# Optimization experiments

Hardware: AMD Instinct MI355X
Metric: run time of the kernel (lower is better)

## Reference

```python
import jax, jax.numpy as jnp
import numpy as np

DECAY = 0.99
EPS = 1e-05
N_EMBED = 4096

def setup_inputs() -> dict:
    key = jax.random.key(0)
    k1, k2 = jax.random.split(key)
    x = jax.random.normal(k1, (32, 1024, 256), dtype=jnp.float32)
    embed = jax.random.normal(k2, (256, N_EMBED), dtype=jnp.float32)
    cluster_size = jnp.zeros((N_EMBED,), dtype=jnp.float32)
    embed_avg = embed  # buffer initialized as embed.clone()
    return {"x": x, "embed": embed, "cluster_size": cluster_size, "embed_avg": embed_avg}

def reference(x, embed, cluster_size, embed_avg):
    # x: [B, L, D]; embed/embed_avg: [D, K]; cluster_size: [K]
    B, L, D = x.shape
    K = embed.shape[1]
    flat = x.reshape(B * L, D)
    dist = (jnp.sum(flat * flat, axis=1, keepdims=True)
            - 2.0 * flat @ embed
            + jnp.sum(embed * embed, axis=0, keepdims=True))
    embed_indices = jnp.argmin(dist, axis=1)  # [N]
    # one-hot scatter-sum (counts per code)
    embed_onehot_sum = jnp.zeros((K,), dtype=x.dtype).at[embed_indices].add(1.0)
    # EMA updates, faithful to the torch source including its quirks:
    #   cluster_size.mul_(decay).add_(onehot_sum, alpha=1-eps)  (note: 1-eps, not 1-decay)
    #   embed_avg.mul_(decay).add(embed_sum, ...)  -> .add (not in-place), so embed_sum is discarded
    cluster_size_new = cluster_size * DECAY + embed_onehot_sum * (1.0 - EPS)
    embed_avg_new = embed_avg * DECAY
    n = jnp.sum(cluster_size_new)
    cs = (cluster_size_new + EPS) / (n + K * EPS) * n  # Laplace-smoothed counts
    embed_new = embed_avg_new / cs[None, :]  # [D, K], copied into self.embed before lookup
    # codebook lookup with the UPDATED embed (matches embed.data.copy_ ordering)
    quantize = embed_new.T[embed_indices].reshape(B, L, D)
    diff = jnp.mean(jnp.square(jax.lax.stop_gradient(quantize) - x))
    quantize_st = x + jax.lax.stop_gradient(quantize - x)  # straight-through
    return (quantize_st, embed_indices.reshape(B, L), diff,
            cluster_size_new, embed_avg_new, embed_new)
```

## Files before the change

### kernel.cpp

```cpp
#include <hip/hip_runtime.h>
#include <math.h>

constexpr float DECAY = 0.99f;
constexpr float EPS_F = 1e-5f;
constexpr float MARGIN = 0.08f;

typedef short bf16x8 __attribute__((ext_vector_type(8)));
typedef float f32x4 __attribute__((ext_vector_type(4)));
typedef float vf4 __attribute__((ext_vector_type(4)));

#define BM 128
#define KSPLIT 2
#define NU 128
#define D_FIX 256

__device__ __forceinline__ unsigned rne_bf16(float f) {
  unsigned u = __float_as_uint(f);
  return (u + 0x7fffu + ((u >> 16) & 1u)) >> 16;
}
__device__ __forceinline__ unsigned pack_hilo(float v) {
  unsigned u = __float_as_uint(v);
  unsigned hi = u & 0xffff0000u;
  float rem = v - __uint_as_float(hi);
  return hi | rne_bf16(rem);
}

__global__ void k_prepack(const float* __restrict__ e, ushort* __restrict__ phl, int K) {
  __shared__ ushort tile[8192];
  const int unit = blockIdx.x;
  const int ct = unit >> 2, du = unit & 3;
  const int t = threadIdx.x;
#pragma unroll
  for (int p = 0; p < 16; ++p) {
    int idx = t + p * 256;
    int dl = idx >> 6, col = idx & 63;
    float v = e[(size_t)(du * 64 + dl) * K + ct * 64 + col];
    unsigned pk = pack_hilo(v);
    int pos = col * 64 + (((dl >> 3) ^ (col & 7)) << 3) + (dl & 7);
    tile[pos] = (ushort)(pk >> 16);
    tile[4096 + pos] = (ushort)(pk & 0xffffu);
  }
  __syncthreads();
  uint4* dst = (uint4*)(phl + (size_t)unit * 8192);
  const uint4* srcT = (const uint4*)tile;
#pragma unroll
  for (int p = 0; p < 4; ++p) dst[t + p * 256] = srcT[t + p * 256];
}

__global__ void k_enorm(const float* __restrict__ e, double* __restrict__ e2d,
                        float* __restrict__ e2f, int D, int K) {
  __shared__ double red[4][64];
  const int kl = threadIdx.x & 63;
  const int part = threadIdx.x >> 6;
  const int k = blockIdx.x * 64 + kl;
  double s = 0.0;
  for (int d = part; d < D; d += 4) {
    double v = (double)e[(size_t)d * K + k];
    s = fma(v, v, s);
  }
  red[part][kl] = s;
  __syncthreads();
  if (part == 0) {
    double t = ((red[0][kl] + red[1][kl]) + red[2][kl]) + red[3][kl];
    e2d[k] = t;
    e2f[k] = (float)t;
  }
}

__launch_bounds__(256, 2)
__global__ void k_argmin_mfma(const float* __restrict__ x, const ushort* __restrict__ phl,
                              const float* __restrict__ e2f,
                              float* __restrict__ bestv, float* __restrict__ secv,
                              int* __restrict__ besti, int N, int K) {
  __shared__ ushort es[2][8192];
  __shared__ float e2s[2048];

  const int tid = threadIdx.x;
  const int w   = tid >> 6;
  const int l   = tid & 63;
  const int g   = l >> 4;
  const int c16 = l & 15;

  const int bflat = blockIdx.x + gridDim.x * blockIdx.y;
  const int xcd   = bflat & 7;
  const int slot  = bflat >> 3;
  const int ytile = xcd >> 2;
  const int xtile = (xcd & 3) * (gridDim.x >> 2) + slot;

  const int kbase = ytile * (K / KSPLIT);
  const int rowW  = xtile * BM + w * 32;

  char* esb = (char*)es;

#define STAGE(u_, b_) do {                                                          \
    const char* gs_ = (const char*)phl +                                            \
        (((size_t)ytile * NU + (size_t)(u_)) << 14) + (w << 12) + (l << 4);         \
    char* ld_ = esb + ((b_) << 14) + (w << 12);                                     \
    __builtin_amdgcn_global_load_lds((const unsigned*)(gs_),        (unsigned*)(ld_),        16, 0, 0); \
    __builtin_amdgcn_global_load_lds((const unsigned*)(gs_ + 1024), (unsigned*)(ld_ + 1024), 16, 0, 0); \
    __builtin_amdgcn_global_load_lds((const unsigned*)(gs_ + 2048), (unsigned*)(ld_ + 2048), 16, 0, 0); \
    __builtin_amdgcn_global_load_lds((const unsigned*)(gs_ + 3072), (unsigned*)(ld_ + 3072), 16, 0, 0); \
  } while (0)

  STAGE(0, 0);

  for (int i = tid; i < 2048; i += 256) e2s[i] = e2f[kbase + i];

  bf16x8 xh[2][8], xl[2][8];
#pragma unroll
  for (int m = 0; m < 2; ++m) {
    const float* xr = x + (size_t)(rowW + m * 16 + c16) * D_FIX + 8 * g;
#pragma unroll
    for (int t = 0; t < 8; ++t) {
      vf4 fa = __builtin_nontemporal_load((const vf4*)(xr + t * 32));
      vf4 fb = __builtin_nontemporal_load((const vf4*)(xr + t * 32 + 4));
      float f[8] = {fa.x, fa.y, fa.z, fa.w, fb.x, fb.y, fb.z, fb.w};
      union { unsigned u[4]; bf16x8 v; } H, L;
#pragma unroll
      for (int p = 0; p < 4; ++p) {
        unsigned w0 = pack_hilo(f[2 * p]);
        unsigned w1 = pack_hilo(f[2 * p + 1]);
        H.u[p] = (w0 >> 16) | (w1 & 0xffff0000u);
        L.u[p] = (w0 & 0xffffu) | (w1 << 16);
      }
      xh[m][t] = H.v;
      xl[m][t] = L.v;
    }
  }

  float best[2][4], sec[2][4];
  int bidx[2][4];
#pragma unroll
  for (int m = 0; m < 2; ++m)
#pragma unroll
    for (int r = 0; r < 4; ++r) { best[m][r] = 3e38f; sec[m][r] = 3e38f; bidx[m][r] = 0; }

  const int sw16 = ((g ^ (c16 & 7)) << 4);
  const char* thr0 = esb + c16 * 128;

  f32x4 acc[2][4];

  for (int u = 0; u < NU; ++u) {
    __syncthreads();
    if (u + 1 < NU) STAGE(u + 1, (u + 1) & 1);
    const int kt = u >> 2, du = u & 3;

    if (du == 0) {
#pragma unroll
      for (int m = 0; m < 2; ++m)
#pragma unroll
        for (int c = 0; c < 4; ++c) acc[m][c] = (f32x4){0.f, 0.f, 0.f, 0.f};
    }

    const char* pbuf = thr0 + ((u & 1) << 14);
#pragma unroll
    for (int tt = 0; tt < 2; ++tt) {
      const int t = 2 * du + tt;
      const char* pt = pbuf + (sw16 ^ (tt << 6));
#pragma unroll
      for (int c = 0; c < 4; ++c) {
        bf16x8 bh = *(const bf16x8*)(pt + c * 2048);
        bf16x8 bl = *(const bf16x8*)(pt + c * 2048 + 8192);
#pragma unroll
        for (int m = 0; m < 2; ++m) {
          acc[m][c] = __builtin_amdgcn_mfma_f32_16x16x32_bf16(xh[m][t], bh, acc[m][c], 0, 0, 0);
          acc[m][c] = __builtin_amdgcn_mfma_f32_16x16x32_bf16(xh[m][t], bl, acc[m][c], 0, 0, 0);
          acc[m][c] = __builtin_amdgcn_mfma_f32_16x16x32_bf16(xl[m][t], bh, acc[m][c], 0, 0, 0);
        }
      }
    }

    if (du == 3) {
#pragma unroll
      for (int c = 0; c < 4; ++c) {
        const int klocal = kt * 64 + c * 16 + c16;
        const float e2v = e2s[klocal];
        const int kg = kbase + klocal;
#pragma unroll
        for (int m = 0; m < 2; ++m)
#pragma unroll
          for (int r = 0; r < 4; ++r) {
            float dist = fmaf(-2.f, acc[m][c][r], e2v);
            if (dist < best[m][r]) { sec[m][r] = best[m][r]; best[m][r] = dist; bidx[m][r] = kg; }
            else sec[m][r] = fminf(sec[m][r], dist);
          }
      }
    }
  }
#undef STAGE

#pragma unroll
  for (int off = 1; off < 16; off <<= 1) {
#pragma unroll
    for (int m = 0; m < 2; ++m)
#pragma unroll
      for (int r = 0; r < 4; ++r) {
        float ob = __shfl_xor(best[m][r], off);
        float os = __shfl_xor(sec[m][r], off);
        int   oi = __shfl_xor(bidx[m][r], off);
        if (ob < best[m][r] || (ob == best[m][r] && oi < bidx[m][r])) {
          sec[m][r] = fminf(best[m][r], os); best[m][r] = ob; bidx[m][r] = oi;
        } else {
          sec[m][r] = fminf(sec[m][r], ob);
        }
      }
  }

  if (c16 == 0) {
    const size_t base = (size_t)ytile * N;
#pragma unroll
    for (int m = 0; m < 2; ++m)
#pragma unroll
      for (int r = 0; r < 4; ++r) {
        int row = rowW + m * 16 + 4 * g + r;
        bestv[base + row] = best[m][r];
        secv[base + row]  = sec[m][r];
        besti[base + row] = bidx[m][r];
      }
  }
}

__global__ void k_combine(const float* __restrict__ bestv, const float* __restrict__ secv,
                          const int* __restrict__ besti, int* __restrict__ idx_out,
                          int* __restrict__ list, unsigned int* __restrict__ count, int N) {
  int n = blockIdx.x * blockDim.x + threadIdx.x;
  if (n >= N) return;
  float b = bestv[n], s = secv[n];
  int bi = besti[n];
#pragma unroll
  for (int p = 1; p < KSPLIT; ++p) {
    float ob = bestv[(size_t)p * N + n];
    float os = secv[(size_t)p * N + n];
    int   oi = besti[(size_t)p * N + n];
    if (ob < b || (ob == b && oi < bi)) { s = fminf(b, os); b = ob; bi = oi; }
    else s = fminf(s, ob);
  }
  idx_out[n] = bi;
  if (s - b < MARGIN) {
    unsigned int p = atomicAdd(count, 1u);
    list[p] = n;
  }
}

__launch_bounds__(256, 4)
__global__ void k_rescan(const float* __restrict__ x, const float* __restrict__ e,
                         const double* __restrict__ e2d, const int* __restrict__ list,
                         const unsigned int* __restrict__ count, int* __restrict__ idx_out,
                         int K) {
  __shared__ double xrow[D_FIX];
  __shared__ double rv[256];
  __shared__ int ri[256];
  const int tid = threadIdx.x;
  const unsigned int cnt = *count;
  for (unsigned int ii = blockIdx.x; ii < cnt; ii += gridDim.x) {
    const int row = list[ii];
    __syncthreads();
    xrow[tid] = (double)x[(size_t)row * D_FIX + tid];
    __syncthreads();
    double bb = 1e300; int bi = 0;
    for (int j = 0; j < K; j += 256) {
      const int k = j + tid;
      const float* ek = e + k;
      double a0 = 0.0, a1 = 0.0, a2 = 0.0, a3 = 0.0;
#pragma unroll 8
      for (int d = 0; d < D_FIX; d += 4) {
        a0 = fma(xrow[d + 0], (double)ek[(size_t)(d + 0) * K], a0);
        a1 = fma(xrow[d + 1], (double)ek[(size_t)(d + 1) * K], a1);
        a2 = fma(xrow[d + 2], (double)ek[(size_t)(d + 2) * K], a2);
        a3 = fma(xrow[d + 3], (double)ek[(size_t)(d + 3) * K], a3);
      }
      double dist = e2d[k] - 2.0 * ((a0 + a1) + (a2 + a3));
      if (dist < bb || (dist == bb && k < bi)) { bb = dist; bi = k; }
    }
    rv[tid] = bb; ri[tid] = bi;
    __syncthreads();
    for (int off = 128; off > 0; off >>= 1) {
      if (tid < off) {
        if (rv[tid + off] < rv[tid] || (rv[tid + off] == rv[tid] && ri[tid + off] < ri[tid])) {
          rv[tid] = rv[tid + off]; ri[tid] = ri[tid + off];
        }
      }
      __syncthreads();
    }
    if (tid == 0) idx_out[row] = ri[0];
    __syncthreads();
  }
}

__global__ void k_hist(const int* __restrict__ idx, unsigned int* __restrict__ cnt,
                       float* __restrict__ idxf_out, int N) {
  int n = blockIdx.x * blockDim.x + threadIdx.x;
  if (n >= N) return;
  int c = idx[n];
  idxf_out[n] = (float)c;
  atomicAdd(&cnt[c], 1u);
}

__global__ void k_cluster(const float* __restrict__ cs_in,
                          const unsigned int* __restrict__ cnt,
                          float* __restrict__ out_csn, float* __restrict__ cs_ws,
                          int K) {
  __shared__ double red[256];
  const int tid = threadIdx.x;
  double s = 0.0;
  for (int k = tid; k < K; k += 256) {
    float csn = cs_in[k] * DECAY + (float)cnt[k] * (1.0f - EPS_F);
    out_csn[k] = csn;
    s += (double)csn;
  }
  red[tid] = s;
  __syncthreads();
  for (int off = 128; off > 0; off >>= 1) {
    if (tid < off) red[tid] += red[tid + off];
    __syncthreads();
  }
  const float n = (float)red[0];
  const float denom = n + (float)K * EPS_F;
  for (int k = tid; k < K; k += 256) {
    float csn = out_csn[k];
    cs_ws[k] = (csn + EPS_F) / denom * n;
  }
}

__global__ void k_embed(const float* __restrict__ avg_in, const float* __restrict__ cs_ws,
                        float* __restrict__ out_avg, float* __restrict__ out_emb, int K) {
  int k = blockIdx.x * blockDim.x + threadIdx.x;
  int d = blockIdx.y;
  if (k >= K) return;
  size_t i = (size_t)d * K + k;
  float a = avg_in[i] * DECAY;
  out_avg[i] = a;
  out_emb[i] = a / cs_ws[k];
}

__global__ void k_transpose(const float* __restrict__ src, float* __restrict__ dst,
                            int D, int K) {
  __shared__ float t[64][65];
  const int kb = blockIdx.x * 64;
  const int db = blockIdx.y * 64;
  const int c = threadIdx.x & 63;
  const int r0 = (threadIdx.x >> 6) * 16;
  for (int i = 0; i < 16; ++i)
    t[r0 + i][c] = src[(size_t)(db + r0 + i) * K + kb + c];
  __syncthreads();
  for (int i = 0; i < 16; ++i)
    dst[(size_t)(kb + r0 + i) * D + db + c] = t[c][r0 + i];
}

__global__ void k_gather(const float* __restrict__ x, const float* __restrict__ embT,
                         const int* __restrict__ idx, float* __restrict__ out_q,
                         float* __restrict__ partial) {
  __shared__ float red[256];
  const int tid = threadIdx.x;
  const int n0 = blockIdx.x * 64;
  float s = 0.f;
  for (int u = 0; u < 16; ++u) {
    int i = u * 256 + tid;
    int row = n0 + (i >> 6);
    int f4 = (i & 63) * 4;
    int code = idx[row];
    float4 q  = *(const float4*)&embT[(size_t)code * D_FIX + f4];
    float4 xv = *(const float4*)&x[(size_t)row * D_FIX + f4];
    float4 dv = {q.x - xv.x, q.y - xv.y, q.z - xv.z, q.w - xv.w};
    float4 val = {xv.x + dv.x, xv.y + dv.y, xv.z + dv.z, xv.w + dv.w};
    *(float4*)&out_q[(size_t)row * D_FIX + f4] = val;
    s += dv.x * dv.x + dv.y * dv.y + dv.z * dv.z + dv.w * dv.w;
  }
  red[tid] = s;
  __syncthreads();
  for (int off = 128; off > 0; off >>= 1) {
    if (tid < off) red[tid] += red[tid + off];
    __syncthreads();
  }
  if (tid == 0) partial[blockIdx.x] = red[0];
}

__global__ void k_diff(const float* __restrict__ partial, float* __restrict__ out_diff,
                       int NB, long long total) {
  __shared__ double red[256];
  const int tid = threadIdx.x;
  double s = 0.0;
  for (int i = tid; i < NB; i += 256) s += (double)partial[i];
  red[tid] = s;
  __syncthreads();
  for (int off = 128; off > 0; off >>= 1) {
    if (tid < off) red[tid] += red[tid + off];
    __syncthreads();
  }
  if (tid == 0) out_diff[0] = (float)(red[0] / (double)total);
}

extern "C" void kernel_launch(void* const* d_in, const int* in_sizes, int n_in,
                              void* d_out, int out_size, void* d_ws, size_t ws_size,
                              hipStream_t stream) {
  const float* x            = (const float*)d_in[0];
  const float* embed        = (const float*)d_in[1];
  const float* cluster_size = (const float*)d_in[2];
  const float* embed_avg    = (const float*)d_in[3];

  const int K = in_sizes[2];
  const int D = in_sizes[1] / K;
  const int N = in_sizes[0] / D;

  float* out      = (float*)d_out;
  float* out_q    = out;
  float* out_idx  = out_q + (size_t)N * D;
  float* out_diff = out_idx + N;
  float* out_csn  = out_diff + 1;
  float* out_avg  = out_csn + K;
  float* out_emb  = out_avg + (size_t)D * K;

  char* ws = (char*)d_ws;
  double*       e2d     = (double*)ws;               ws += (size_t)K * 8;
  float*        e2f     = (float*)ws;                ws += (size_t)K * 4;
  int*          idx     = (int*)ws;                  ws += (size_t)N * 4;
  unsigned int* cnt     = (unsigned int*)ws;         ws += (size_t)K * 4;
  float*        cs_ws   = (float*)ws;                ws += (size_t)K * 4;
  float*        partial = (float*)ws;                ws += (size_t)(N / 64) * 4;
  float*        bestv   = (float*)ws;                ws += (size_t)KSPLIT * N * 4;
  float*        secv    = (float*)ws;                ws += (size_t)KSPLIT * N * 4;
  int*          besti   = (int*)ws;                  ws += (size_t)KSPLIT * N * 4;
  int*          list    = (int*)ws;                  ws += (size_t)N * 4;
  unsigned int* count   = (unsigned int*)ws;         ws += 64;
  float*        embT    = (float*)ws;                ws += (size_t)K * D * 4;
  ushort*       phl     = (ushort*)ws;               ws += (size_t)K * D * 4;

  hipMemsetAsync(cnt, 0, (size_t)K * sizeof(unsigned int), stream);
  hipMemsetAsync(count, 0, sizeof(unsigned int), stream);

  k_prepack<<<dim3((K / 64) * 4), dim3(256), 0, stream>>>(embed, phl, K);
  k_enorm<<<dim3(K / 64), dim3(256), 0, stream>>>(embed, e2d, e2f, D, K);
  k_argmin_mfma<<<dim3(N / BM, KSPLIT), dim3(256), 0, stream>>>(x, phl, e2f, bestv, secv,
                                                                besti, N, K);
  k_combine<<<dim3((N + 255) / 256), dim3(256), 0, stream>>>(bestv, secv, besti, idx,
                                                             list, count, N);
  k_rescan<<<dim3(1024), dim3(256), 0, stream>>>(x, embed, e2d, list, count, idx, K);
  k_hist<<<dim3((N + 255) / 256), dim3(256), 0, stream>>>(idx, cnt, out_idx, N);
  k_cluster<<<dim3(1), dim3(256), 0, stream>>>(cluster_size, cnt, out_csn, cs_ws, K);
  k_embed<<<dim3((K + 255) / 256, D), dim3(256), 0, stream>>>(embed_avg, cs_ws, out_avg, out_emb, K);
  k_transpose<<<dim3(K / 64, D / 64), dim3(256), 0, stream>>>(out_emb, embT, D, K);
  k_gather<<<dim3(N / 64), dim3(256), 0, stream>>>(x, embT, idx, out_q, partial);
  k_diff<<<dim3(1), dim3(256), 0, stream>>>(partial, out_diff, N / 64, (long long)N * D);
}
```

Before: 510.3 us.

## Deepen argmin pipeline, widen blocks, and fuse auxiliary kernels

The MFMA argmin kernel now uses 512-thread blocks covering 256 rows and a 6-deep LDS ring with explicit vmcnt waits instead of double buffering, so more codebook tiles are in flight. Prepack and norm are merged into one kernel, the histogram is folded into combine and rescan, and the embed update is fused with the transpose. The packed codebook now lives in the out_avg output region instead of separate workspace, relying on it being overwritten later. These changes cut kernel launches and extra passes, at the cost of larger LDS use and tighter correctness dependencies on the buffer-reuse ordering.

```diff
diff --git a/kernel.cpp b/kernel.cpp
--- a/kernel.cpp
+++ b/kernel.cpp
@@ -9,9 +9,10 @@
 typedef float f32x4 __attribute__((ext_vector_type(4)));
 typedef float vf4 __attribute__((ext_vector_type(4)));
 
-#define BM 128
+#define BM 256
 #define KSPLIT 2
 #define NU 128
+#define NBUF 6
 #define D_FIX 256
 
 __device__ __forceinline__ unsigned rne_bf16(float f) {
@@ -25,59 +26,58 @@
   return hi | rne_bf16(rem);
 }
 
-__global__ void k_prepack(const float* __restrict__ e, ushort* __restrict__ phl, int K) {
+__global__ void k_prepack_enorm(const float* __restrict__ e, ushort* __restrict__ phl,
+                                double* __restrict__ e2d, float* __restrict__ e2f, int K) {
   __shared__ ushort tile[8192];
-  const int unit = blockIdx.x;
-  const int ct = unit >> 2, du = unit & 3;
+  __shared__ double red[4][64];
+  const int ct = blockIdx.x;
   const int t = threadIdx.x;
-#pragma unroll
-  for (int p = 0; p < 16; ++p) {
-    int idx = t + p * 256;
-    int dl = idx >> 6, col = idx & 63;
-    float v = e[(size_t)(du * 64 + dl) * K + ct * 64 + col];
-    unsigned pk = pack_hilo(v);
-    int pos = col * 64 + (((dl >> 3) ^ (col & 7)) << 3) + (dl & 7);
-    tile[pos] = (ushort)(pk >> 16);
-    tile[4096 + pos] = (ushort)(pk & 0xffffu);
-  }
-  __syncthreads();
-  uint4* dst = (uint4*)(phl + (size_t)unit * 8192);
-  const uint4* srcT = (const uint4*)tile;
-#pragma unroll
-  for (int p = 0; p < 4; ++p) dst[t + p * 256] = srcT[t + p * 256];
-}
-
-__global__ void k_enorm(const float* __restrict__ e, double* __restrict__ e2d,
-                        float* __restrict__ e2f, int D, int K) {
-  __shared__ double red[4][64];
-  const int kl = threadIdx.x & 63;
-  const int part = threadIdx.x >> 6;
-  const int k = blockIdx.x * 64 + kl;
+  for (int du = 0; du < 4; ++du) {
+    __syncthreads();
+#pragma unroll
+    for (int p = 0; p < 16; ++p) {
+      int idx = t + p * 256;
+      int dl = idx >> 6, col = idx & 63;
+      float v = e[(size_t)(du * 64 + dl) * K + ct * 64 + col];
+      unsigned pk = pack_hilo(v);
+      int pos = col * 64 + (((dl >> 3) ^ (col & 7)) << 3) + (dl & 7);
+      tile[pos] = (ushort)(pk >> 16);
+      tile[4096 + pos] = (ushort)(pk & 0xffffu);
+    }
+    __syncthreads();
+    uint4* dst = (uint4*)(phl + (size_t)(ct * 4 + du) * 8192);
+    const uint4* srcT = (const uint4*)tile;
+#pragma unroll
+    for (int p = 0; p < 4; ++p) dst[t + p * 256] = srcT[t + p * 256];
+  }
+  const int kl = t & 63;
+  const int part = t >> 6;
+  const int k = ct * 64 + kl;
   double s = 0.0;
-  for (int d = part; d < D; d += 4) {
+  for (int d = part; d < D_FIX; d += 4) {
     double v = (double)e[(size_t)d * K + k];
     s = fma(v, v, s);
   }
   red[part][kl] = s;
   __syncthreads();
   if (part == 0) {
-    double t = ((red[0][kl] + red[1][kl]) + red[2][kl]) + red[3][kl];
-    e2d[k] = t;
-    e2f[k] = (float)t;
-  }
-}
-
-__launch_bounds__(256, 2)
+    double tt = ((red[0][kl] + red[1][kl]) + red[2][kl]) + red[3][kl];
+    e2d[k] = tt;
+    e2f[k] = (float)tt;
+  }
+}
+
+__launch_bounds__(512, 2)
 __global__ void k_argmin_mfma(const float* __restrict__ x, const ushort* __restrict__ phl,
                               const float* __restrict__ e2f,
                               float* __restrict__ bestv, float* __restrict__ secv,
                               int* __restrict__ besti, int N, int K) {
-  __shared__ ushort es[2][8192];
+  __shared__ ushort es[NBUF][8192];
   __shared__ float e2s[2048];
 
   const int tid = threadIdx.x;
+  const int l   = tid & 63;
   const int w   = tid >> 6;
-  const int l   = tid & 63;
   const int g   = l >> 4;
   const int c16 = l & 15;
 
@@ -91,20 +91,16 @@
   const int rowW  = xtile * BM + w * 32;
 
   char* esb = (char*)es;
-
-#define STAGE(u_, b_) do {                                                          \
-    const char* gs_ = (const char*)phl +                                            \
-        (((size_t)ytile * NU + (size_t)(u_)) << 14) + (w << 12) + (l << 4);         \
-    char* ld_ = esb + ((b_) << 14) + (w << 12);                                     \
-    __builtin_amdgcn_global_load_lds((const unsigned*)(gs_),        (unsigned*)(ld_),        16, 0, 0); \
-    __builtin_amdgcn_global_load_lds((const unsigned*)(gs_ + 1024), (unsigned*)(ld_ + 1024), 16, 0, 0); \
-    __builtin_amdgcn_global_load_lds((const unsigned*)(gs_ + 2048), (unsigned*)(ld_ + 2048), 16, 0, 0); \
-    __builtin_amdgcn_global_load_lds((const unsigned*)(gs_ + 3072), (unsigned*)(ld_ + 3072), 16, 0, 0); \
-  } while (0)
-
-  STAGE(0, 0);
-
-  for (int i = tid; i < 2048; i += 256) e2s[i] = e2f[kbase + i];
+  const size_t unit0 = (size_t)ytile * NU;
+
+  auto stage = [&](int u) {
+    const char* gs = (const char*)phl + ((unit0 + (size_t)u) << 14) + (w << 11) + (l << 4);
+    char* ld = esb + ((u % NBUF) << 14) + (w << 11) + (l << 4);
+    __builtin_amdgcn_global_load_lds((const unsigned*)gs,          (unsigned*)ld,          16, 0, 0);
+    __builtin_amdgcn_global_load_lds((const unsigned*)(gs + 1024), (unsigned*)(ld + 1024), 16, 0, 0);
+  };
+
+  for (int i = tid; i < 2048; i += 512) e2s[i] = e2f[kbase + i];
 
   bf16x8 xh[2][8], xl[2][8];
 #pragma unroll
@@ -136,23 +132,19 @@
     for (int r = 0; r < 4; ++r) { best[m][r] = 3e38f; sec[m][r] = 3e38f; bidx[m][r] = 0; }
 
   const int sw16 = ((g ^ (c16 & 7)) << 4);
-  const char* thr0 = esb + c16 * 128;
+  const int c16x128 = c16 * 128;
 
   f32x4 acc[2][4];
 
-  for (int u = 0; u < NU; ++u) {
-    __syncthreads();
-    if (u + 1 < NU) STAGE(u + 1, (u + 1) & 1);
+  auto compute = [&](int u) {
     const int kt = u >> 2, du = u & 3;
-
     if (du == 0) {
 #pragma unroll
       for (int m = 0; m < 2; ++m)
 #pragma unroll
         for (int c = 0; c < 4; ++c) acc[m][c] = (f32x4){0.f, 0.f, 0.f, 0.f};
     }
-
-    const char* pbuf = thr0 + ((u & 1) << 14);
+    const char* pbuf = esb + ((u % NBUF) << 14) + c16x128;
 #pragma unroll
     for (int tt = 0; tt < 2; ++tt) {
       const int t = 2 * du + tt;
@@ -169,7 +161,6 @@
         }
       }
     }
-
     if (du == 3) {
 #pragma unroll
       for (int c = 0; c < 4; ++c) {
@@ -186,8 +177,32 @@
           }
       }
     }
-  }
-#undef STAGE
+  };
+
+  __syncthreads();
+  stage(0); stage(1); stage(2); stage(3); stage(4);
+
+  for (int u = 0; u < NU - 5; ++u) {
+    asm volatile("s_waitcnt vmcnt(8)" ::: "memory");
+    __builtin_amdgcn_s_barrier();
+    stage(u + 5);
+    compute(u);
+  }
+  asm volatile("s_waitcnt vmcnt(8)" ::: "memory");
+  __builtin_amdgcn_s_barrier();
+  compute(NU - 5);
+  asm volatile("s_waitcnt vmcnt(6)" ::: "memory");
+  __builtin_amdgcn_s_barrier();
+  compute(NU - 4);
+  asm volatile("s_waitcnt vmcnt(4)" ::: "memory");
+  __builtin_amdgcn_s_barrier();
+  compute(NU - 3);
+  asm volatile("s_waitcnt vmcnt(2)" ::: "memory");
+  __builtin_amdgcn_s_barrier();
+  compute(NU - 2);
+  asm volatile("s_waitcnt vmcnt(0)" ::: "memory");
+  __builtin_amdgcn_s_barrier();
+  compute(NU - 1);
 
 #pragma unroll
   for (int off = 1; off < 16; off <<= 1) {
@@ -222,6 +237,7 @@
 
 __global__ void k_combine(const float* __restrict__ bestv, const float* __restrict__ secv,
                           const int* __restrict__ besti, int* __restrict__ idx_out,
+                          float* __restrict__ idxf_out, unsigned int* __restrict__ cnt,
                           int* __restrict__ list, unsigned int* __restrict__ count, int N) {
   int n = blockIdx.x * blockDim.x + threadIdx.x;
   if (n >= N) return;
@@ -236,9 +252,12 @@
     else s = fminf(s, ob);
   }
   idx_out[n] = bi;
+  idxf_out[n] = (float)bi;
   if (s - b < MARGIN) {
     unsigned int p = atomicAdd(count, 1u);
     list[p] = n;
+  } else {
+    atomicAdd(&cnt[bi], 1u);
   }
 }
 
@@ -246,13 +265,14 @@
 __global__ void k_rescan(const float* __restrict__ x, const float* __restrict__ e,
                          const double* __restrict__ e2d, const int* __restrict__ list,
                          const unsigned int* __restrict__ count, int* __restrict__ idx_out,
+                         float* __restrict__ idxf_out, unsigned int* __restrict__ cnt,
                          int K) {
   __shared__ double xrow[D_FIX];
   __shared__ double rv[256];
   __shared__ int ri[256];
   const int tid = threadIdx.x;
-  const unsigned int cnt = *count;
-  for (unsigned int ii = blockIdx.x; ii < cnt; ii += gridDim.x) {
+  const unsigned int cntN = *count;
+  for (unsigned int ii = blockIdx.x; ii < cntN; ii += gridDim.x) {
     const int row = list[ii];
     __syncthreads();
     xrow[tid] = (double)x[(size_t)row * D_FIX + tid];
@@ -282,18 +302,13 @@
       }
       __syncthreads();
     }
-    if (tid == 0) idx_out[row] = ri[0];
-    __syncthreads();
-  }
-}
-
-__global__ void k_hist(const int* __restrict__ idx, unsigned int* __restrict__ cnt,
-                       float* __restrict__ idxf_out, int N) {
-  int n = blockIdx.x * blockDim.x + threadIdx.x;
-  if (n >= N) return;
-  int c = idx[n];
-  idxf_out[n] = (float)c;
-  atomicAdd(&cnt[c], 1u);
+    if (tid == 0) {
+      idx_out[row] = ri[0];
+      idxf_out[row] = (float)ri[0];
+      atomicAdd(&cnt[ri[0]], 1u);
+    }
+    __syncthreads();
+  }
 }
 
 __global__ void k_cluster(const float* __restrict__ cs_in,
@@ -322,29 +337,26 @@
   }
 }
 
-__global__ void k_embed(const float* __restrict__ avg_in, const float* __restrict__ cs_ws,
-                        float* __restrict__ out_avg, float* __restrict__ out_emb, int K) {
-  int k = blockIdx.x * blockDim.x + threadIdx.x;
-  int d = blockIdx.y;
-  if (k >= K) return;
-  size_t i = (size_t)d * K + k;
-  float a = avg_in[i] * DECAY;
-  out_avg[i] = a;
-  out_emb[i] = a / cs_ws[k];
-}
-
-__global__ void k_transpose(const float* __restrict__ src, float* __restrict__ dst,
-                            int D, int K) {
-  __shared__ float t[64][65];
+__global__ void k_embed2(const float* __restrict__ avg_in, const float* __restrict__ cs_ws,
+                         float* __restrict__ out_avg, float* __restrict__ out_emb,
+                         float* __restrict__ embT, int D, int K) {
+  __shared__ float tr[64][65];
   const int kb = blockIdx.x * 64;
   const int db = blockIdx.y * 64;
   const int c = threadIdx.x & 63;
   const int r0 = (threadIdx.x >> 6) * 16;
+  const float csv = cs_ws[kb + c];
+  for (int i = 0; i < 16; ++i) {
+    size_t off = (size_t)(db + r0 + i) * K + kb + c;
+    float a = avg_in[off] * DECAY;
+    out_avg[off] = a;
+    float emb = a / csv;
+    out_emb[off] = emb;
+    tr[r0 + i][c] = emb;
+  }
+  __syncthreads();
   for (int i = 0; i < 16; ++i)
-    t[r0 + i][c] = src[(size_t)(db + r0 + i) * K + kb + c];
-  __syncthreads();
-  for (int i = 0; i < 16; ++i)
-    dst[(size_t)(kb + r0 + i) * D + db + c] = t[c][r0 + i];
+    embT[(size_t)(kb + r0 + i) * D + db + c] = tr[c][r0 + i];
 }
 
 __global__ void k_gather(const float* __restrict__ x, const float* __restrict__ embT,
@@ -410,6 +422,8 @@
   float* out_avg  = out_csn + K;
   float* out_emb  = out_avg + (size_t)D * K;
 
+  ushort* phl = (ushort*)out_avg;
+
   char* ws = (char*)d_ws;
   double*       e2d     = (double*)ws;               ws += (size_t)K * 8;
   float*        e2f     = (float*)ws;                ws += (size_t)K * 4;
@@ -423,22 +437,20 @@
   int*          list    = (int*)ws;                  ws += (size_t)N * 4;
   unsigned int* count   = (unsigned int*)ws;         ws += 64;
   float*        embT    = (float*)ws;                ws += (size_t)K * D * 4;
-  ushort*       phl     = (ushort*)ws;               ws += (size_t)K * D * 4;
 
   hipMemsetAsync(cnt, 0, (size_t)K * sizeof(unsigned int), stream);
   hipMemsetAsync(count, 0, sizeof(unsigned int), stream);
 
-  k_prepack<<<dim3((K / 64) * 4), dim3(256), 0, stream>>>(embed, phl, K);
-  k_enorm<<<dim3(K / 64), dim3(256), 0, stream>>>(embed, e2d, e2f, D, K);
-  k_argmin_mfma<<<dim3(N / BM, KSPLIT), dim3(256), 0, stream>>>(x, phl, e2f, bestv, secv,
+  k_prepack_enorm<<<dim3(K / 64), dim3(256), 0, stream>>>(embed, phl, e2d, e2f, K);
+  k_argmin_mfma<<<dim3(N / BM, KSPLIT), dim3(512), 0, stream>>>(x, phl, e2f, bestv, secv,
                                                                 besti, N, K);
   k_combine<<<dim3((N + 255) / 256), dim3(256), 0, stream>>>(bestv, secv, besti, idx,
-                                                             list, count, N);
-  k_rescan<<<dim3(1024), dim3(256), 0, stream>>>(x, embed, e2d, list, count, idx, K);
-  k_hist<<<dim3((N + 255) / 256), dim3(256), 0, stream>>>(idx, cnt, out_idx, N);
+                                                             out_idx, cnt, list, count, N);
+  k_rescan<<<dim3(1024), dim3(256), 0, stream>>>(x, embed, e2d, list, count, idx,
+                                                 out_idx, cnt, K);
   k_cluster<<<dim3(1), dim3(256), 0, stream>>>(cluster_size, cnt, out_csn, cs_ws, K);
-  k_embed<<<dim3((K + 255) / 256, D), dim3(256), 0, stream>>>(embed_avg, cs_ws, out_avg, out_emb, K);
-  k_transpose<<<dim3(K / 64, D / 64), dim3(256), 0, stream>>>(out_emb, embT, D, K);
+  k_embed2<<<dim3(K / 64, D / 64), dim3(256), 0, stream>>>(embed_avg, cs_ws, out_avg,
+                                                           out_emb, embT, D, K);
   k_gather<<<dim3(N / 64), dim3(256), 0, stream>>>(x, embT, idx, out_q, partial);
   k_diff<<<dim3(1), dim3(256), 0, stream>>>(partial, out_diff, N / 64, (long long)N * D);
 }
```

Result: no change. 512.9 us (+0.5%).
